# Kernel tuning notes

Measured on AMD Instinct MI355X. Metric: run time of the kernel, lower is better.

Reference implementation:

```python
import jax, jax.numpy as jnp
import numpy as np

N_NODES = 10000
N_EDGES = 320000


def gcn_conv(x, edge_index, edge_weight, W, b):
    """PyG GCNConv (add_self_loops=True, normalize=True) with edge weights.
    x: [N, Fin], edge_index: [2, E] (row=source, col=target), W: [Fin, Fout].
    """
    n = x.shape[0]
    row, col = edge_index[0], edge_index[1]
    # add self-loops with weight 1
    loop = jnp.arange(n, dtype=edge_index.dtype)
    row = jnp.concatenate([row, loop])
    col = jnp.concatenate([col, loop])
    ew = jnp.concatenate([edge_weight, jnp.ones((n,), dtype=edge_weight.dtype)])
    # symmetric normalization: D^-1/2 A D^-1/2
    deg = jax.ops.segment_sum(ew, col, num_segments=n)
    dinv = jnp.where(deg > 0, jax.lax.rsqrt(deg), 0.0)
    norm = dinv[row] * ew * dinv[col]  # [E+N]
    # linear transform first (smaller of the two widths often), then aggregate
    xw = x @ W  # [N, Fout]
    msg = norm[:, None] * xw[row]  # [E+N, Fout] gather
    out = jax.ops.segment_sum(msg, col, num_segments=n)  # scatter-add
    return out + b


def setup_inputs() -> dict:
    key = jax.random.key(0)
    ks = jax.random.split(key, 8)
    F = 256
    x = jax.random.normal(ks[0], (N_NODES, F), dtype=jnp.float32)
    edge_index = jax.random.randint(ks[1], (2, N_EDGES), 0, N_NODES, dtype=jnp.int64)
    edge_weights = jax.random.uniform(ks[2], (N_EDGES,), dtype=jnp.float32)
    s1 = 1.0 / np.sqrt(F)
    s2 = 1.0 / np.sqrt(2 * F)
    s3 = 1.0 / np.sqrt(3 * F)
    W1 = jax.random.normal(ks[3], (F, 2 * F), dtype=jnp.float32) * s1
    b1 = jnp.zeros((2 * F,), dtype=jnp.float32)
    W2 = jax.random.normal(ks[4], (2 * F, 3 * F), dtype=jnp.float32) * s2
    b2 = jnp.zeros((3 * F,), dtype=jnp.float32)
    W3 = jax.random.normal(ks[5], (3 * F, 8), dtype=jnp.float32) * s3
    b3 = jnp.zeros((8,), dtype=jnp.float32)
    return {"x": x, "edge_index": edge_index, "edge_weights": edge_weights,
            "W1": W1, "b1": b1, "W2": W2, "b2": b2, "W3": W3, "b3": b3}


def reference(x, edge_index, edge_weights, W1, b1, W2, b2, W3, b3):
    h = jax.nn.relu(gcn_conv(x, edge_index, edge_weights, W1, b1))
    h = jax.nn.relu(gcn_conv(h, edge_index, edge_weights, W2, b2))
    return gcn_conv(h, edge_index, edge_weights, W3, b3)
```

## Files before the change

### kernel.cpp

```cpp
#include <hip/hip_runtime.h>

#define N_NODES 10000
#define N_EDGES 320000
#define E_PAD (N_EDGES + 8 * N_NODES)

__device__ __forceinline__ unsigned short f2h_bits(float v) {
    _Float16 h = (_Float16)v;
    unsigned short u;
    __builtin_memcpy(&u, &h, 2);
    return u;
}
__device__ __forceinline__ float h2f_lo(unsigned int g) {
    unsigned short u = (unsigned short)(g & 0xFFFFu);
    _Float16 h; __builtin_memcpy(&h, &u, 2);
    return (float)h;
}
__device__ __forceinline__ float h2f_hi(unsigned int g) {
    unsigned short u = (unsigned short)(g >> 16);
    _Float16 h; __builtin_memcpy(&h, &u, 2);
    return (float)h;
}

__global__ __launch_bounds__(256) void setup_kernel(
        float* __restrict__ deg, int* __restrict__ counts,
        int* __restrict__ csr_src, float* __restrict__ csr_w,
        const float* __restrict__ x, unsigned short* __restrict__ xh,
        const float* __restrict__ W1, unsigned short* __restrict__ w1t,
        const float* __restrict__ W2, unsigned short* __restrict__ w2t) {
    int i = blockIdx.x * 256 + threadIdx.x;
    const int S0 = N_NODES;
    const int S1 = S0 + E_PAD;
    const int S2 = S1 + N_NODES * 256;
    const int S3 = S2 + 256 * 512;
    const int S4 = S3 + 512 * 768;
    if (i < S0) {
        deg[i] = 1.0f; counts[i] = 0;
    } else if (i < S1) {
        int j = i - S0;
        csr_src[j] = 0; csr_w[j] = 0.f;
    } else if (i < S2) {
        int j = i - S1;
        xh[j] = f2h_bits(x[j]);
    } else if (i < S3) {
        int j = i - S2;
        int k = j >> 9, n = j & 511;
        w1t[n * 256 + k] = f2h_bits(W1[j]);
    } else if (i < S4) {
        int j = i - S3;
        int k = j / 768, n = j - k * 768;
        w2t[n * 512 + k] = f2h_bits(W2[j]);
    }
}

__global__ __launch_bounds__(256) void count_slot_kernel(const int* __restrict__ col,
                                                         const float* __restrict__ ew,
                                                         float* __restrict__ deg,
                                                         int* __restrict__ counts,
                                                         int* __restrict__ slot, int e) {
    int i = blockIdx.x * 256 + threadIdx.x;
    if (i < e) {
        int c = col[i];
        slot[i] = atomicAdd(counts + c, 1);
        atomicAdd(deg + c, ew[i]);
    }
}

__global__ __launch_bounds__(1024) void scan_dinv_kernel(const int* __restrict__ counts,
                                                         int* __restrict__ ptr,
                                                         const float* __restrict__ deg,
                                                         float* __restrict__ dinv, int n) {
    __shared__ int wsum[16];
    __shared__ int woff[16];
    const int t = (int)threadIdx.x;
    const int lane = t & 63;
    const int wid = t >> 6;
    const int base = t * 10;
    int loc[10];
    int tot = 0;
#pragma unroll
    for (int q = 0; q < 10; ++q) {
        int i = base + q;
        int v = 0;
        if (i < n) {
            v = (counts[i] + 7) & ~7;
            float d = deg[i];
            dinv[i] = (d > 0.0f) ? rsqrtf(d) : 0.0f;
        }
        loc[q] = tot;
        tot += v;
    }
    int x = tot;
#pragma unroll
    for (int off = 1; off < 64; off <<= 1) {
        int u = __shfl_up(x, off);
        if (lane >= off) x += u;
    }
    if (lane == 63) wsum[wid] = x;
    __syncthreads();
    if (wid == 0 && lane < 16) {
        int s = wsum[lane];
        int y = s;
#pragma unroll
        for (int off = 1; off < 16; off <<= 1) {
            int u = __shfl_up(y, off);
            if (lane >= off) y += u;
        }
        woff[lane] = y - s;
        if (lane == 15) ptr[n] = y;
    }
    __syncthreads();
    const int tbase = woff[wid] + (x - tot);
#pragma unroll
    for (int q = 0; q < 10; ++q) {
        int i = base + q;
        if (i < n) ptr[i] = tbase + loc[q];
    }
}

__global__ __launch_bounds__(256) void scatter_kernel(const int* __restrict__ row,
                                                      const int* __restrict__ col,
                                                      const float* __restrict__ ew,
                                                      const float* __restrict__ dinv,
                                                      const int* __restrict__ ptr,
                                                      const int* __restrict__ slot,
                                                      int* __restrict__ csr_src,
                                                      float* __restrict__ csr_w, int e) {
    int i = blockIdx.x * 256 + threadIdx.x;
    if (i < e) {
        int c = col[i], r = row[i];
        int pos = ptr[c] + slot[i];
        csr_src[pos] = r;
        csr_w[pos] = dinv[r] * ew[i] * dinv[c];
    }
}

template <int F, int SSHIFT>
__global__ __launch_bounds__(64) void agg_slice_kernel(const unsigned int* __restrict__ xpk,
                                                       const int* __restrict__ ptr,
                                                       const int* __restrict__ csr_src,
                                                       const float* __restrict__ csr_w,
                                                       const float* __restrict__ dinv,
                                                       unsigned int* __restrict__ o) {
    constexpr int F2 = F / 2;
    const int b = blockIdx.x;
    const int slice = b & ((1 << SSHIFT) - 1);
    const int node = b >> SSHIFT;
    const int f2 = slice * 64 + (int)threadIdx.x;
    const float di = dinv[node];
    const float si = di * di;
    unsigned int gs = xpk[node * F2 + f2];
    float acc0 = si * h2f_lo(gs);
    float acc1 = si * h2f_hi(gs);
    const int s = ptr[node], e = ptr[node + 1];

    for (int j = s; j < e; j += 8) {
        int s0 = csr_src[j + 0], s1 = csr_src[j + 1], s2 = csr_src[j + 2], s3 = csr_src[j + 3];
        int s4 = csr_src[j + 4], s5 = csr_src[j + 5], s6 = csr_src[j + 6], s7 = csr_src[j + 7];
        float w0 = csr_w[j + 0], w1 = csr_w[j + 1], w2 = csr_w[j + 2], w3 = csr_w[j + 3];
        float w4 = csr_w[j + 4], w5 = csr_w[j + 5], w6 = csr_w[j + 6], w7 = csr_w[j + 7];
        unsigned int g0 = xpk[s0 * F2 + f2];
        unsigned int g1 = xpk[s1 * F2 + f2];
        unsigned int g2 = xpk[s2 * F2 + f2];
        unsigned int g3 = xpk[s3 * F2 + f2];
        unsigned int g4 = xpk[s4 * F2 + f2];
        unsigned int g5 = xpk[s5 * F2 + f2];
        unsigned int g6 = xpk[s6 * F2 + f2];
        unsigned int g7 = xpk[s7 * F2 + f2];
        acc0 += w0 * h2f_lo(g0) + w1 * h2f_lo(g1) + w2 * h2f_lo(g2) + w3 * h2f_lo(g3);
        acc1 += w0 * h2f_hi(g0) + w1 * h2f_hi(g1) + w2 * h2f_hi(g2) + w3 * h2f_hi(g3);
        acc0 += w4 * h2f_lo(g4) + w5 * h2f_lo(g5) + w6 * h2f_lo(g6) + w7 * h2f_lo(g7);
        acc1 += w4 * h2f_hi(g4) + w5 * h2f_hi(g5) + w6 * h2f_hi(g6) + w7 * h2f_hi(g7);
    }

    unsigned short h0 = f2h_bits(acc0);
    unsigned short h1 = f2h_bits(acc1);
    o[node * F2 + f2] = ((unsigned int)h1 << 16) | h0;
}

typedef _Float16 half8 __attribute__((ext_vector_type(8)));
typedef float f32x4 __attribute__((ext_vector_type(4)));

#define TM 128
#define TN 128
#define BK 32
#define LDS_A 0
#define LDS_B 8192
#define LDS_BUF 16384

__device__ __forceinline__ void async16(const unsigned short* g, unsigned char* l) {
    __builtin_amdgcn_global_load_lds(
        (const __attribute__((address_space(1))) unsigned int*)g,
        (__attribute__((address_space(3))) unsigned int*)l, 16, 0, 0);
}

__global__ __launch_bounds__(256, 3) void gemm_mfma_kernel(
        const unsigned short* __restrict__ A,
        const unsigned short* __restrict__ Bt,
        const float* __restrict__ bias,
        unsigned short* __restrict__ Cb,
        int M, int K, int N) {
    __shared__ unsigned char lds[2 * LDS_BUF];
    const int t = (int)threadIdx.x;

    const int gx = (int)gridDim.x;
    const int nwg = gx * (int)gridDim.y;
    const int lin = (int)blockIdx.y * gx + (int)blockIdx.x;
    const int xcd = lin & 7, idx = lin >> 3;
    const int q = nwg >> 3, r = nwg & 7;
    const int logi = (xcd < r ? xcd * (q + 1) : r * (q + 1) + (xcd - r) * q) + idx;
    const int bm = (logi / gx) * TM;
    const int bn = (logi % gx) * TN;

    const int lane = t & 63;
    const int wave = t >> 6;
    const int wm = (wave & 1) * 64;
    const int wn = (wave >> 1) * 64;

    const int slr = lane >> 2;
    const int scc = (lane & 3) ^ ((slr >> 1) & 3);
    const int bi0 = wave * 2, bi1 = wave * 2 + 1;
    const unsigned short* gA0 = A + (size_t)(bm + bi0 * 16 + slr) * K + scc * 8;
    const unsigned short* gA1 = A + (size_t)(bm + bi1 * 16 + slr) * K + scc * 8;
    const unsigned short* gB0 = Bt + (size_t)(bn + bi0 * 16 + slr) * K + scc * 8;
    const unsigned short* gB1 = Bt + (size_t)(bn + bi1 * 16 + slr) * K + scc * 8;

    const int quad = lane >> 4;
    const int lr16 = lane & 15;
    const int fs = (quad ^ ((lr16 >> 1) & 3)) * 16;

    f32x4 acc[4][4];
    const f32x4 zero4 = {0.f, 0.f, 0.f, 0.f};
#pragma unroll
    for (int i = 0; i < 4; ++i)
#pragma unroll
        for (int j = 0; j < 4; ++j) acc[i][j] = zero4;

    const int KT = K / BK;

    auto stage = [&](int kt, int buf) {
        const int k0 = kt * BK;
        unsigned char* b = &lds[buf * LDS_BUF];
        async16(gA0 + k0, b + LDS_A + bi0 * 1024);
        async16(gA1 + k0, b + LDS_A + bi1 * 1024);
        async16(gB0 + k0, b + LDS_B + bi0 * 1024);
        async16(gB1 + k0, b + LDS_B + bi1 * 1024);
    };

    stage(0, 0);
    __syncthreads();

    for (int kt = 0; kt < KT; ++kt) {
        const int buf = kt & 1;
        if (kt + 1 < KT) stage(kt + 1, buf ^ 1);

        unsigned char* b = &lds[buf * LDS_BUF];
        half8 av[4], bv[4];
#pragma unroll
        for (int i = 0; i < 4; ++i) {
            int ro = (wm + i * 16 + lr16) * 64 + fs;
            av[i] = *(const half8*)(b + LDS_A + ro);
        }
#pragma unroll
        for (int j = 0; j < 4; ++j) {
            int ro = (wn + j * 16 + lr16) * 64 + fs;
            bv[j] = *(const half8*)(b + LDS_B + ro);
        }
#pragma unroll
        for (int i = 0; i < 4; ++i)
#pragma unroll
            for (int j = 0; j < 4; ++j)
                acc[i][j] = __builtin_amdgcn_mfma_f32_16x16x32_f16(av[i], bv[j], acc[i][j], 0, 0, 0);
        __syncthreads();
    }

    float bcol[4];
#pragma unroll
    for (int j = 0; j < 4; ++j) bcol[j] = bias[bn + wn + j * 16 + lr16];
#pragma unroll
    for (int i = 0; i < 4; ++i) {
#pragma unroll
        for (int r2 = 0; r2 < 4; ++r2) {
            int m = bm + wm + i * 16 + quad * 4 + r2;
            if (m < M) {
#pragma unroll
                for (int j = 0; j < 4; ++j) {
                    float vv = fmaxf(acc[i][j][r2] + bcol[j], 0.f);
                    Cb[(size_t)m * N + bn + wn + j * 16 + lr16] = f2h_bits(vv);
                }
            }
        }
    }
}

__global__ __launch_bounds__(64) void gemm_n8_kernel(const unsigned int* __restrict__ Apk,
                                                     const float* __restrict__ B,
                                                     float* __restrict__ C) {
    const int m = blockIdx.x;
    const int lane = (int)threadIdx.x;
    const unsigned int* a = Apk + m * 384;
    float acc[8] = {};
#pragma unroll
    for (int it = 0; it < 6; ++it) {
        int j2 = lane + it * 64;
        unsigned int av = a[j2];
        float a0 = h2f_lo(av), a1 = h2f_hi(av);
        const float* B0 = B + (size_t)(2 * j2) * 8;
        float4 p0 = *(const float4*)(B0);
        float4 p1 = *(const float4*)(B0 + 4);
        float4 q0 = *(const float4*)(B0 + 8);
        float4 q1 = *(const float4*)(B0 + 12);
        acc[0] += a0 * p0.x + a1 * q0.x; acc[1] += a0 * p0.y + a1 * q0.y;
        acc[2] += a0 * p0.z + a1 * q0.z; acc[3] += a0 * p0.w + a1 * q0.w;
        acc[4] += a0 * p1.x + a1 * q1.x; acc[5] += a0 * p1.y + a1 * q1.y;
        acc[6] += a0 * p1.z + a1 * q1.z; acc[7] += a0 * p1.w + a1 * q1.w;
    }
#pragma unroll
    for (int off = 32; off > 0; off >>= 1) {
#pragma unroll
        for (int i = 0; i < 8; ++i) acc[i] += __shfl_down(acc[i], off);
    }
    if (lane == 0) {
#pragma unroll
        for (int i = 0; i < 8; ++i) C[(size_t)m * 8 + i] = acc[i];
    }
}

__global__ __launch_bounds__(64) void agg8_kernel(const float* __restrict__ xw,
                                                  const int* __restrict__ ptr,
                                                  const int* __restrict__ csr_src,
                                                  const float* __restrict__ csr_w,
                                                  const float* __restrict__ dinv,
                                                  const float* __restrict__ bias,
                                                  float* __restrict__ out) {
    int node = blockIdx.x;
    int lane = threadIdx.x;
    float acc[8] = {};
    int s = ptr[node], e = ptr[node + 1];
    for (int j = s + lane; j < e; j += 64) {
        int src = csr_src[j];
        float w = csr_w[j];
        float4 g0 = *(const float4*)(xw + (size_t)src * 8);
        float4 g1 = *(const float4*)(xw + (size_t)src * 8 + 4);
        acc[0] += w * g0.x; acc[1] += w * g0.y; acc[2] += w * g0.z; acc[3] += w * g0.w;
        acc[4] += w * g1.x; acc[5] += w * g1.y; acc[6] += w * g1.z; acc[7] += w * g1.w;
    }
#pragma unroll
    for (int off = 32; off > 0; off >>= 1) {
#pragma unroll
        for (int i = 0; i < 8; ++i) acc[i] += __shfl_down(acc[i], off);
    }
    if (lane == 0) {
        float di = dinv[node];
        float si = di * di;
#pragma unroll
        for (int i = 0; i < 8; ++i)
            out[(size_t)node * 8 + i] = acc[i] + si * xw[(size_t)node * 8 + i] + bias[i];
    }
}


extern "C" void kernel_launch(void* const* d_in, const int* in_sizes, int n_in,
                              void* d_out, int out_size, void* d_ws, size_t ws_size,
                              hipStream_t stream) {
    const int N = N_NODES, E = N_EDGES;
    const int N_PAD = ((N + TM - 1) / TM) * TM;
    const float* x   = (const float*)d_in[0];
    const int*   ei  = (const int*)d_in[1];
    const float* ew  = (const float*)d_in[2];
    const float* W1  = (const float*)d_in[3];
    const float* b1  = (const float*)d_in[4];
    const float* W2  = (const float*)d_in[5];
    const float* b2  = (const float*)d_in[6];
    const float* W3  = (const float*)d_in[7];
    const float* b3  = (const float*)d_in[8];
    float* out = (float*)d_out;

    const int* row = ei;
    const int* col = ei + E;

    char* ws = (char*)d_ws;
    size_t off = 0;
    auto alloc = [&](size_t bytes) {
        void* p = ws + off;
        off += (bytes + 255) & ~(size_t)255;
        return p;
    };
    float*          deg     = (float*)alloc((size_t)N * 4);
    float*          dinv    = (float*)alloc((size_t)N * 4);
    int*            counts  = (int*)alloc((size_t)N * 4);
    int*            col_ptr = (int*)alloc((size_t)(N + 1) * 4);
    int*            slot    = (int*)alloc((size_t)E * 4);
    int*            csr_src = (int*)alloc((size_t)E_PAD * 4);
    float*          csr_w   = (float*)alloc((size_t)E_PAD * 4);
    unsigned short* xh      = (unsigned short*)alloc((size_t)N * 256 * 2);
    unsigned short* h1h     = (unsigned short*)alloc((size_t)N * 512 * 2);
    unsigned short* h2h     = (unsigned short*)alloc((size_t)N * 768 * 2);
    unsigned short* Aagg    = (unsigned short*)alloc((size_t)N_PAD * 512 * 2);
    unsigned short* W1t     = (unsigned short*)alloc((size_t)512 * 256 * 2);
    unsigned short* W2t     = (unsigned short*)alloc((size_t)768 * 512 * 2);
    float*          xw8     = (float*)alloc((size_t)N * 8 * 4);
    (void)ws_size;

    int nb_edges = (E + 255) / 256;

    {
        int tot = N + E_PAD + N * 256 + 256 * 512 + 512 * 768;
        setup_kernel<<<(tot + 255) / 256, 256, 0, stream>>>(
            deg, counts, csr_src, csr_w, x, xh, W1, W1t, W2, W2t);
    }
    count_slot_kernel<<<nb_edges, 256, 0, stream>>>(col, ew, deg, counts, slot, E);
    scan_dinv_kernel<<<1, 1024, 0, stream>>>(counts, col_ptr, deg, dinv, N);
    scatter_kernel<<<nb_edges, 256, 0, stream>>>(row, col, ew, dinv, col_ptr, slot,
                                                 csr_src, csr_w, E);

    agg_slice_kernel<256, 1><<<N * 2, 64, 0, stream>>>(
        (const unsigned int*)xh, col_ptr, csr_src, csr_w, dinv, (unsigned int*)Aagg);
    {
        dim3 grid(512 / TN, N_PAD / TM);
        gemm_mfma_kernel<<<grid, 256, 0, stream>>>(Aagg, W1t, b1, h1h, N, 256, 512);
    }
    agg_slice_kernel<512, 2><<<N * 4, 64, 0, stream>>>(
        (const unsigned int*)h1h, col_ptr, csr_src, csr_w, dinv, (unsigned int*)Aagg);
    {
        dim3 grid(768 / TN, N_PAD / TM);
        gemm_mfma_kernel<<<grid, 256, 0, stream>>>(Aagg, W2t, b2, h2h, N, 512, 768);
    }
    gemm_n8_kernel<<<N, 64, 0, stream>>>((const unsigned int*)h2h, W3, xw8);
    agg8_kernel<<<N, 64, 0, stream>>>(xw8, col_ptr, csr_src, csr_w, dinv, b3, out);

    (void)out_size; (void)n_in; (void)in_sizes;
}
```

Before: 231.8 us.

## Pack four waves per block, vectorize CSR loads, drop slot array via atomicSub

```diff
diff --git a/kernel.cpp b/kernel.cpp
--- a/kernel.cpp
+++ b/kernel.cpp
@@ -52,15 +52,14 @@
     }
 }
 
-__global__ __launch_bounds__(256) void count_slot_kernel(const int* __restrict__ col,
-                                                         const float* __restrict__ ew,
-                                                         float* __restrict__ deg,
-                                                         int* __restrict__ counts,
-                                                         int* __restrict__ slot, int e) {
+__global__ __launch_bounds__(256) void count_kernel(const int* __restrict__ col,
+                                                    const float* __restrict__ ew,
+                                                    float* __restrict__ deg,
+                                                    int* __restrict__ counts, int e) {
     int i = blockIdx.x * 256 + threadIdx.x;
     if (i < e) {
         int c = col[i];
-        slot[i] = atomicAdd(counts + c, 1);
+        atomicAdd(counts + c, 1);
         atomicAdd(deg + c, ew[i]);
     }
 }
@@ -122,30 +121,32 @@
                                                       const float* __restrict__ ew,
                                                       const float* __restrict__ dinv,
                                                       const int* __restrict__ ptr,
-                                                      const int* __restrict__ slot,
+                                                      int* __restrict__ counts,
                                                       int* __restrict__ csr_src,
                                                       float* __restrict__ csr_w, int e) {
     int i = blockIdx.x * 256 + threadIdx.x;
     if (i < e) {
         int c = col[i], r = row[i];
-        int pos = ptr[c] + slot[i];
+        int sl = atomicSub(counts + c, 1) - 1;
+        int pos = ptr[c] + sl;
         csr_src[pos] = r;
         csr_w[pos] = dinv[r] * ew[i] * dinv[c];
     }
 }
 
 template <int F, int SSHIFT>
-__global__ __launch_bounds__(64) void agg_slice_kernel(const unsigned int* __restrict__ xpk,
-                                                       const int* __restrict__ ptr,
-                                                       const int* __restrict__ csr_src,
-                                                       const float* __restrict__ csr_w,
-                                                       const float* __restrict__ dinv,
-                                                       unsigned int* __restrict__ o) {
+__global__ __launch_bounds__(256, 8) void agg_slice_kernel(const unsigned int* __restrict__ xpk,
+                                                           const int* __restrict__ ptr,
+                                                           const int* __restrict__ csr_src,
+                                                           const float* __restrict__ csr_w,
+                                                           const float* __restrict__ dinv,
+                                                           unsigned int* __restrict__ o) {
     constexpr int F2 = F / 2;
-    const int b = blockIdx.x;
-    const int slice = b & ((1 << SSHIFT) - 1);
-    const int node = b >> SSHIFT;
-    const int f2 = slice * 64 + (int)threadIdx.x;
+    const int unit = __builtin_amdgcn_readfirstlane((int)blockIdx.x * 4 + ((int)threadIdx.x >> 6));
+    const int slice = unit & ((1 << SSHIFT) - 1);
+    const int node = unit >> SSHIFT;
+    const int lane = (int)threadIdx.x & 63;
+    const int f2 = slice * 64 + lane;
     const float di = dinv[node];
     const float si = di * di;
     unsigned int gs = xpk[node * F2 + f2];
@@ -153,23 +154,58 @@
     float acc1 = si * h2f_hi(gs);
     const int s = ptr[node], e = ptr[node + 1];
 
-    for (int j = s; j < e; j += 8) {
-        int s0 = csr_src[j + 0], s1 = csr_src[j + 1], s2 = csr_src[j + 2], s3 = csr_src[j + 3];
-        int s4 = csr_src[j + 4], s5 = csr_src[j + 5], s6 = csr_src[j + 6], s7 = csr_src[j + 7];
-        float w0 = csr_w[j + 0], w1 = csr_w[j + 1], w2 = csr_w[j + 2], w3 = csr_w[j + 3];
-        float w4 = csr_w[j + 4], w5 = csr_w[j + 5], w6 = csr_w[j + 6], w7 = csr_w[j + 7];
-        unsigned int g0 = xpk[s0 * F2 + f2];
-        unsigned int g1 = xpk[s1 * F2 + f2];
-        unsigned int g2 = xpk[s2 * F2 + f2];
-        unsigned int g3 = xpk[s3 * F2 + f2];
-        unsigned int g4 = xpk[s4 * F2 + f2];
-        unsigned int g5 = xpk[s5 * F2 + f2];
-        unsigned int g6 = xpk[s6 * F2 + f2];
-        unsigned int g7 = xpk[s7 * F2 + f2];
-        acc0 += w0 * h2f_lo(g0) + w1 * h2f_lo(g1) + w2 * h2f_lo(g2) + w3 * h2f_lo(g3);
-        acc1 += w0 * h2f_hi(g0) + w1 * h2f_hi(g1) + w2 * h2f_hi(g2) + w3 * h2f_hi(g3);
-        acc0 += w4 * h2f_lo(g4) + w5 * h2f_lo(g5) + w6 * h2f_lo(g6) + w7 * h2f_lo(g7);
-        acc1 += w4 * h2f_hi(g4) + w5 * h2f_hi(g5) + w6 * h2f_hi(g6) + w7 * h2f_hi(g7);
+    int j = s;
+    for (; j + 16 <= e; j += 16) {
+        int4   sa = *(const int4*)(csr_src + j);
+        int4   sb = *(const int4*)(csr_src + j + 4);
+        int4   sc = *(const int4*)(csr_src + j + 8);
+        int4   sd = *(const int4*)(csr_src + j + 12);
+        float4 wa = *(const float4*)(csr_w + j);
+        float4 wb = *(const float4*)(csr_w + j + 4);
+        float4 wc = *(const float4*)(csr_w + j + 8);
+        float4 wd = *(const float4*)(csr_w + j + 12);
+        unsigned int g0 = xpk[sa.x * F2 + f2];
+        unsigned int g1 = xpk[sa.y * F2 + f2];
+        unsigned int g2 = xpk[sa.z * F2 + f2];
+        unsigned int g3 = xpk[sa.w * F2 + f2];
+        unsigned int g4 = xpk[sb.x * F2 + f2];
+        unsigned int g5 = xpk[sb.y * F2 + f2];
+        unsigned int g6 = xpk[sb.z * F2 + f2];
+        unsigned int g7 = xpk[sb.w * F2 + f2];
+        unsigned int g8 = xpk[sc.x * F2 + f2];
+        unsigned int g9 = xpk[sc.y * F2 + f2];
+        unsigned int gA = xpk[sc.z * F2 + f2];
+        unsigned int gB = xpk[sc.w * F2 + f2];
+        unsigned int gC = xpk[sd.x * F2 + f2];
+        unsigned int gD = xpk[sd.y * F2 + f2];
+        unsigned int gE = xpk[sd.z * F2 + f2];
+        unsigned int gF = xpk[sd.w * F2 + f2];
+        acc0 += wa.x * h2f_lo(g0) + wa.y * h2f_lo(g1) + wa.z * h2f_lo(g2) + wa.w * h2f_lo(g3);
+        acc1 += wa.x * h2f_hi(g0) + wa.y * h2f_hi(g1) + wa.z * h2f_hi(g2) + wa.w * h2f_hi(g3);
+        acc0 += wb.x * h2f_lo(g4) + wb.y * h2f_lo(g5) + wb.z * h2f_lo(g6) + wb.w * h2f_lo(g7);
+        acc1 += wb.x * h2f_hi(g4) + wb.y * h2f_hi(g5) + wb.z * h2f_hi(g6) + wb.w * h2f_hi(g7);
+        acc0 += wc.x * h2f_lo(g8) + wc.y * h2f_lo(g9) + wc.z * h2f_lo(gA) + wc.w * h2f_lo(gB);
+        acc1 += wc.x * h2f_hi(g8) + wc.y * h2f_hi(g9) + wc.z * h2f_hi(gA) + wc.w * h2f_hi(gB);
+        acc0 += wd.x * h2f_lo(gC) + wd.y * h2f_lo(gD) + wd.z * h2f_lo(gE) + wd.w * h2f_lo(gF);
+        acc1 += wd.x * h2f_hi(gC) + wd.y * h2f_hi(gD) + wd.z * h2f_hi(gE) + wd.w * h2f_hi(gF);
+    }
+    if (j < e) {
+        int4   sa = *(const int4*)(csr_src + j);
+        int4   sb = *(const int4*)(csr_src + j + 4);
+        float4 wa = *(const float4*)(csr_w + j);
+        float4 wb = *(const float4*)(csr_w + j + 4);
+        unsigned int g0 = xpk[sa.x * F2 + f2];
+        unsigned int g1 = xpk[sa.y * F2 + f2];
+        unsigned int g2 = xpk[sa.z * F2 + f2];
+        unsigned int g3 = xpk[sa.w * F2 + f2];
+        unsigned int g4 = xpk[sb.x * F2 + f2];
+        unsigned int g5 = xpk[sb.y * F2 + f2];
+        unsigned int g6 = xpk[sb.z * F2 + f2];
+        unsigned int g7 = xpk[sb.w * F2 + f2];
+        acc0 += wa.x * h2f_lo(g0) + wa.y * h2f_lo(g1) + wa.z * h2f_lo(g2) + wa.w * h2f_lo(g3);
+        acc1 += wa.x * h2f_hi(g0) + wa.y * h2f_hi(g1) + wa.z * h2f_hi(g2) + wa.w * h2f_hi(g3);
+        acc0 += wb.x * h2f_lo(g4) + wb.y * h2f_lo(g5) + wb.z * h2f_lo(g6) + wb.w * h2f_lo(g7);
+        acc1 += wb.x * h2f_hi(g4) + wb.y * h2f_hi(g5) + wb.z * h2f_hi(g6) + wb.w * h2f_hi(g7);
     }
 
     unsigned short h0 = f2h_bits(acc0);
@@ -292,11 +328,11 @@
     }
 }
 
-__global__ __launch_bounds__(64) void gemm_n8_kernel(const unsigned int* __restrict__ Apk,
-                                                     const float* __restrict__ B,
-                                                     float* __restrict__ C) {
-    const int m = blockIdx.x;
-    const int lane = (int)threadIdx.x;
+__global__ __launch_bounds__(256) void gemm_n8_kernel(const unsigned int* __restrict__ Apk,
+                                                      const float* __restrict__ B,
+                                                      float* __restrict__ C) {
+    const int m = __builtin_amdgcn_readfirstlane((int)blockIdx.x * 4 + ((int)threadIdx.x >> 6));
+    const int lane = (int)threadIdx.x & 63;
     const unsigned int* a = Apk + m * 384;
     float acc[8] = {};
 #pragma unroll
@@ -325,15 +361,15 @@
     }
 }
 
-__global__ __launch_bounds__(64) void agg8_kernel(const float* __restrict__ xw,
-                                                  const int* __restrict__ ptr,
-                                                  const int* __restrict__ csr_src,
-                                                  const float* __restrict__ csr_w,
-                                                  const float* __restrict__ dinv,
-                                                  const float* __restrict__ bias,
-                                                  float* __restrict__ out) {
-    int node = blockIdx.x;
-    int lane = threadIdx.x;
+__global__ __launch_bounds__(256) void agg8_kernel(const float* __restrict__ xw,
+                                                   const int* __restrict__ ptr,
+                                                   const int* __restrict__ csr_src,
+                                                   const float* __restrict__ csr_w,
+                                                   const float* __restrict__ dinv,
+                                                   const float* __restrict__ bias,
+                                                   float* __restrict__ out) {
+    const int node = __builtin_amdgcn_readfirstlane((int)blockIdx.x * 4 + ((int)threadIdx.x >> 6));
+    const int lane = (int)threadIdx.x & 63;
     float acc[8] = {};
     int s = ptr[node], e = ptr[node + 1];
     for (int j = s + lane; j < e; j += 64) {
@@ -389,7 +425,6 @@
     float*          dinv    = (float*)alloc((size_t)N * 4);
     int*            counts  = (int*)alloc((size_t)N * 4);
     int*            col_ptr = (int*)alloc((size_t)(N + 1) * 4);
-    int*            slot    = (int*)alloc((size_t)E * 4);
     int*            csr_src = (int*)alloc((size_t)E_PAD * 4);
     float*          csr_w   = (float*)alloc((size_t)E_PAD * 4);
     unsigned short* xh      = (unsigned short*)alloc((size_t)N * 256 * 2);
@@ -408,25 +443,25 @@
         setup_kernel<<<(tot + 255) / 256, 256, 0, stream>>>(
             deg, counts, csr_src, csr_w, x, xh, W1, W1t, W2, W2t);
     }
-    count_slot_kernel<<<nb_edges, 256, 0, stream>>>(col, ew, deg, counts, slot, E);
+    count_kernel<<<nb_edges, 256, 0, stream>>>(col, ew, deg, counts, E);
     scan_dinv_kernel<<<1, 1024, 0, stream>>>(counts, col_ptr, deg, dinv, N);
-    scatter_kernel<<<nb_edges, 256, 0, stream>>>(row, col, ew, dinv, col_ptr, slot,
+    scatter_kernel<<<nb_edges, 256, 0, stream>>>(row, col, ew, dinv, col_ptr, counts,
                                                  csr_src, csr_w, E);
 
-    agg_slice_kernel<256, 1><<<N * 2, 64, 0, stream>>>(
+    agg_slice_kernel<256, 1><<<N * 2 / 4, 256, 0, stream>>>(
         (const unsigned int*)xh, col_ptr, csr_src, csr_w, dinv, (unsigned int*)Aagg);
     {
         dim3 grid(512 / TN, N_PAD / TM);
         gemm_mfma_kernel<<<grid, 256, 0, stream>>>(Aagg, W1t, b1, h1h, N, 256, 512);
     }
-    agg_slice_kernel<512, 2><<<N * 4, 64, 0, stream>>>(
+    agg_slice_kernel<512, 2><<<N * 4 / 4, 256, 0, stream>>>(
         (const unsigned int*)h1h, col_ptr, csr_src, csr_w, dinv, (unsigned int*)Aagg);
     {
         dim3 grid(768 / TN, N_PAD / TM);
         gemm_mfma_kernel<<<grid, 256, 0, stream>>>(Aagg, W2t, b2, h2h, N, 512, 768);
     }
-    gemm_n8_kernel<<<N, 64, 0, stream>>>((const unsigned int*)h2h, W3, xw8);
-    agg8_kernel<<<N, 64, 0, stream>>>(xw8, col_ptr, csr_src, csr_w, dinv, b3, out);
+    gemm_n8_kernel<<<N / 4, 256, 0, stream>>>((const unsigned int*)h2h, W3, xw8);
+    agg8_kernel<<<N / 4, 256, 0, stream>>>(xw8, col_ptr, csr_src, csr_w, dinv, b3, out);
 
     (void)out_size; (void)n_in; (void)in_sizes;
 }
```

After: 253.6 us. 9.4% more time.
